# Kernel optimization log

Hardware: AMD Instinct MI355X
Metric: run time of the kernel (lower is better)

The kernel has to match this reference:

```python
import jax, jax.numpy as jnp
from jax import lax
import numpy as np

B, N = 64, 128           # graphs per batch, nodes per graph
MAX_LEVEL = 3
N_TRUNKS, TRUNK_LEN = 32, 32
H, OUT = 256, 10


def setup_inputs() -> dict:
    key = jax.random.key(0)
    ks = jax.random.split(key, 12)
    batch_feature = jax.random.normal(ks[0], (B, N), dtype=jnp.float32)
    trunk_idx = jax.random.randint(ks[1], (MAX_LEVEL, N_TRUNKS, TRUNK_LEN), 0, N, dtype=jnp.int32)
    trunk_len = jax.random.randint(ks[2], (MAX_LEVEL, N_TRUNKS), 1, TRUNK_LEN + 1, dtype=jnp.int32)
    s = 1.0 / np.sqrt(H)
    W_enc = jax.random.uniform(ks[3], (1, H), jnp.float32, -1.0, 1.0)
    b_enc = jax.random.uniform(ks[4], (H,), jnp.float32, -1.0, 1.0)
    W_ih = jax.random.uniform(ks[5], (MAX_LEVEL, 4 * H, H), jnp.float32, -s, s)
    W_hh = jax.random.uniform(ks[6], (MAX_LEVEL, 4 * H, H), jnp.float32, -s, s)
    b_ih = jax.random.uniform(ks[7], (MAX_LEVEL, 4 * H), jnp.float32, -s, s)
    b_hh = jax.random.uniform(ks[8], (MAX_LEVEL, 4 * H), jnp.float32, -s, s)
    W_lin = jax.random.uniform(ks[9], (MAX_LEVEL, H, OUT), jnp.float32, -s, s)
    b_lin = jax.random.uniform(ks[10], (MAX_LEVEL, OUT), jnp.float32, -s, s)
    return {"batch_feature": batch_feature, "trunk_idx": trunk_idx, "trunk_len": trunk_len,
            "W_enc": W_enc, "b_enc": b_enc, "W_ih": W_ih, "W_hh": W_hh,
            "b_ih": b_ih, "b_hh": b_hh, "W_lin": W_lin, "b_lin": b_lin}


def _lstm_scan(seq, W_ih, W_hh, b):
    """seq: [L, M, H] -> all hidden states [L, M, H] (single-layer LSTM, PyTorch gate order i,f,g,o)."""
    M = seq.shape[1]
    Hd = W_hh.shape[1]
    def step(carry, x_t):
        h, c = carry
        gates = x_t @ W_ih.T + h @ W_hh.T + b   # [M, 4H]
        i, f, g, o = jnp.split(gates, 4, axis=-1)
        c = jax.nn.sigmoid(f) * c + jax.nn.sigmoid(i) * jnp.tanh(g)
        h = jax.nn.sigmoid(o) * jnp.tanh(c)
        return (h, c), h
    init = (jnp.zeros((M, Hd), seq.dtype), jnp.zeros((M, Hd), seq.dtype))
    _, hs = lax.scan(step, init, seq)
    return hs


def reference(batch_feature, trunk_idx, trunk_len, W_enc, b_enc, W_ih, W_hh, b_ih, b_hh, W_lin, b_lin):
    Bv, Nv = batch_feature.shape
    Hd = W_enc.shape[1]
    # node encoder on scalar features: x [B*N, 1] @ W_enc [1, H]
    x_attr = (batch_feature.reshape(-1, 1) @ W_enc + b_enc).reshape(Bv, Nv, Hd)
    trunk_len = jnp.maximum(trunk_len, 1)
    score = jnp.zeros((Bv, W_lin.shape[-1]), x_attr.dtype)
    for l in range(trunk_idx.shape[0]):
        idx = trunk_idx[l]                       # [T, L]
        T, L = idx.shape
        seqs = x_attr[:, idx]                    # gather trunks -> [B, T, L, H]
        seqs = seqs.reshape(Bv * T, L, Hd).transpose(1, 0, 2)   # [L, B*T, H]
        hs = _lstm_scan(seqs, W_ih[l], W_hh[l], b_ih[l] + b_hh[l])  # [L, B*T, H]
        lens = jnp.tile(trunk_len[l], Bv)        # [B*T]
        h_last = hs[lens - 1, jnp.arange(Bv * T)]   # hidden at last valid step (== packed h_n)
        h_trunk = h_last.reshape(Bv, T, Hd).sum(axis=1)  # scatter-sum per graph (indices are i repeated T times)
        score = score + h_trunk @ W_lin[l] + b_lin[l]
    return score


if __name__ == "__main__":
    out = reference(**setup_inputs())
    print(out.shape, out.dtype)
```

## Files before the change

kernel.cpp:

```cpp
#include <hip/hip_runtime.h>
#include <hip/hip_bf16.h>
#include <stdint.h>

#define B_   64
#define N_   128
#define H_   256
#define FH   1024
#define NT   32
#define TL   32
#define LV   3
#define OUT_ 10
#define NTRK 96
#define UNITS 384

typedef __attribute__((ext_vector_type(4))) int   int4v;
typedef __attribute__((ext_vector_type(4))) float f32x4;

#define QW  (0.0625f / 127.0f)
#define QH  (1.0f / 127.0f)
#define QS  (QW * QH)
#define L2E 1.442695041f
#define QSI (-L2E * QS)
#define QSG (2.0f * L2E * QS)
#define C2  (2.0f * L2E)

__device__ inline float exp2f_(float x) { return __builtin_amdgcn_exp2f(x); }
__device__ inline float rcpf_(float x)  { return __builtin_amdgcn_rcpf(x); }

__global__ void prep_all(const float* __restrict__ W_enc, const float* __restrict__ b_enc,
                         const float* __restrict__ W_ih, const float* __restrict__ b_ih,
                         const float* __restrict__ b_hh, const float* __restrict__ W_hh,
                         const float* __restrict__ b_lin, const int* __restrict__ trunk_len,
                         float* __restrict__ u, float* __restrict__ v,
                         char* __restrict__ whh_i8, float* __restrict__ out,
                         int* __restrict__ sorted, int* __restrict__ counter) {
    int blk = blockIdx.x;
    int tid = threadIdx.x;
    if (blk < 768) {
        int j = blk * 4 + (tid >> 6);
        int lane = tid & 63;
        const float4 w  = ((const float4*)(W_ih + (size_t)j * H_))[lane];
        const float4 we = ((const float4*)W_enc)[lane];
        const float4 be = ((const float4*)b_enc)[lane];
        float du = w.x * we.x + w.y * we.y + w.z * we.z + w.w * we.w;
        float dv = w.x * be.x + w.y * be.y + w.z * be.z + w.w * be.w;
        for (int m = 32; m >= 1; m >>= 1) { du += __shfl_xor(du, m); dv += __shfl_xor(dv, m); }
        if (lane == 0) {
            int g = (j & 1023) >> 8;
            float s = (g == 2) ? (2.0f * L2E) : (-L2E);
            u[j] = s * du;
            v[j] = s * (dv + b_ih[j] + b_hh[j]);
        }
    } else if (blk < 1536) {
        int gid = (blk - 768) * 256 + tid;
        const float4 w = ((const float4*)W_hh)[gid];
        char4 o;
        int a0 = __float2int_rn(w.x * (127.0f / 0.0625f));
        int a1 = __float2int_rn(w.y * (127.0f / 0.0625f));
        int a2 = __float2int_rn(w.z * (127.0f / 0.0625f));
        int a3 = __float2int_rn(w.w * (127.0f / 0.0625f));
        a0 = a0 > 127 ? 127 : (a0 < -127 ? -127 : a0);
        a1 = a1 > 127 ? 127 : (a1 < -127 ? -127 : a1);
        a2 = a2 > 127 ? 127 : (a2 < -127 ? -127 : a2);
        a3 = a3 > 127 ? 127 : (a3 < -127 ? -127 : a3);
        o.x = (char)a0; o.y = (char)a1; o.z = (char)a2; o.w = (char)a3;
        ((char4*)whh_i8)[gid] = o;
        if (gid < B_ * OUT_) {
            int oo = gid % OUT_;
            out[gid] = b_lin[oo] + b_lin[OUT_ + oo] + b_lin[2 * OUT_ + oo];
        }
    } else {
        if (tid < NTRK) {
            int li = trunk_len[tid]; if (li < 1) li = 1;
            int rank = 0;
            for (int j2 = 0; j2 < NTRK; ++j2) {
                int lj = trunk_len[j2]; if (lj < 1) lj = 1;
                rank += (lj > li) || (lj == li && j2 < tid);
            }
            sorted[rank] = tid;
        }
        if (tid == 0) *counter = 0;
    }
}

__global__ __launch_bounds__(1024) __attribute__((amdgpu_waves_per_eu(4, 4)))
void lstm_main(const float* __restrict__ bfeat, const int* __restrict__ trunk_idx,
               const int* __restrict__ trunk_len,
               const char* __restrict__ whh_i8,
               const float* __restrict__ u, const float* __restrict__ v,
               const float* __restrict__ W_lin, const int* __restrict__ sorted,
               int* __restrict__ counter, float* __restrict__ out) {
    __shared__ __align__(16) char hbuf[2][16][272];
    __shared__ __align__(16) float sbuf[2][16];
    __shared__ int sh_uid;

    const int tid = threadIdx.x;
    const int w = tid >> 6;
    const int lane = tid & 63;
    const int col = lane & 15;
    const int q = lane >> 4;

    int4v z4; z4[0] = 0; z4[1] = 0; z4[2] = 0; z4[3] = 0;
    asm volatile("" : "+v"(z4));

    for (;;) {
        if (tid == 0) sh_uid = atomicAdd(counter, 1);
        __syncthreads();
        const int uid = sh_uid;
        if (uid >= UNITS) break;

        const int r = uid >> 2, qq = uid & 3;
        const int tt = sorted[r];
        const int l = tt >> 5;
        const int b0 = qq * 16;

        int len = trunk_len[tt];
        if (len < 1) len = 1;
        const int* tix = trunk_idx + tt * TL;
        const char* whh_l = whh_i8 + (size_t)l * FH * H_;

        int4v Breg[4][4];
        #pragma unroll
        for (int g = 0; g < 4; ++g) {
            int j = g * 256 + w * 16 + col;
            const char* bp = whh_l + (size_t)j * H_ + q * 16;
            #pragma unroll
            for (int k = 0; k < 4; ++k)
                Breg[g][k] = *(const int4v*)(bp + k * 64);
        }

        float u_r[4], v_r[4];
        {
            const float* u_l = u + l * FH;
            const float* v_l = v + l * FH;
            #pragma unroll
            for (int g = 0; g < 4; ++g) {
                int j = g * 256 + w * 16 + col;
                u_r[g] = u_l[j];
                v_r[g] = v_l[j];
            }
        }

        #pragma unroll
        for (int g = 0; g < 4; ++g) {
            #pragma unroll
            for (int k = 0; k < 4; ++k)
                asm volatile("" : "+v"(Breg[g][k]));
            asm volatile("" : "+v"(u_r[g]), "+v"(v_r[g]));
        }

        float c_r[4];

        if (tid < 16) sbuf[0][tid] = bfeat[(b0 + tid) * N_ + tix[0]];
        __syncthreads();

        {
            if (len > 1 && tid < 16) sbuf[1][tid] = bfeat[(b0 + tid) * N_ + tix[1]];
            f32x4 sv = *(const f32x4*)&sbuf[0][q * 4];
            #pragma unroll
            for (int rg = 0; rg < 4; ++rg) {
                float xi = fmaf(sv[rg], u_r[0], v_r[0]);
                float xg = fmaf(sv[rg], u_r[2], v_r[2]);
                float xo = fmaf(sv[rg], u_r[3], v_r[3]);
                float si = rcpf_(exp2f_(xi) + 1.0f);
                float so = rcpf_(exp2f_(xo) + 1.0f);
                float tg = fmaf(-2.0f, rcpf_(exp2f_(xg) + 1.0f), 1.0f);
                float cn = si * tg;
                c_r[rg] = cn;
                float th127 = fmaf(-254.0f, rcpf_(exp2f_(C2 * cn) + 1.0f), 127.0f);
                hbuf[1][q * 4 + rg][w * 16 + col] = (char)__float2int_rn(so * th127);
            }
            __syncthreads();
        }

        for (int p = 1; p < len; ++p) {
            const int ri = p & 1, wi = ri ^ 1;

            if (p + 1 < len && tid < 16)
                sbuf[wi][tid] = bfeat[(b0 + tid) * N_ + tix[p + 1]];

            f32x4 sv = *(const f32x4*)&sbuf[ri][q * 4];

            int4v acc[4];
            #pragma unroll
            for (int k = 0; k < 4; ++k) {
                int4v af = *(const int4v*)&hbuf[ri][col][k * 64 + q * 16];
                if (k == 0) {
                    #pragma unroll
                    for (int g = 0; g < 4; ++g)
                        acc[g] = __builtin_amdgcn_mfma_i32_16x16x64_i8(af, Breg[g][0], z4, 0, 0, 0);
                } else {
                    #pragma unroll
                    for (int g = 0; g < 4; ++g)
                        acc[g] = __builtin_amdgcn_mfma_i32_16x16x64_i8(af, Breg[g][k], acc[g], 0, 0, 0);
                }
            }

            #pragma unroll
            for (int rg = 0; rg < 4; ++rg) {
                float xi = fmaf((float)acc[0][rg], QSI, fmaf(sv[rg], u_r[0], v_r[0]));
                float xf = fmaf((float)acc[1][rg], QSI, fmaf(sv[rg], u_r[1], v_r[1]));
                float xg = fmaf((float)acc[2][rg], QSG, fmaf(sv[rg], u_r[2], v_r[2]));
                float xo = fmaf((float)acc[3][rg], QSI, fmaf(sv[rg], u_r[3], v_r[3]));
                float si = rcpf_(exp2f_(xi) + 1.0f);
                float sf = rcpf_(exp2f_(xf) + 1.0f);
                float so = rcpf_(exp2f_(xo) + 1.0f);
                float tg = fmaf(-2.0f, rcpf_(exp2f_(xg) + 1.0f), 1.0f);
                float cn = fmaf(sf, c_r[rg], si * tg);
                c_r[rg] = cn;
                float th127 = fmaf(-254.0f, rcpf_(exp2f_(C2 * cn) + 1.0f), 127.0f);
                hbuf[wi][q * 4 + rg][w * 16 + col] = (char)__float2int_rn(so * th127);
            }

            __syncthreads();
        }

        const char (*hl)[272] = hbuf[len & 1];
        const float* wl = W_lin + l * H_ * OUT_;
        if (tid < 16 * OUT_) {
            int m = tid / OUT_, o = tid % OUT_;
            float s = 0.f;
            for (int k = 0; k < H_; ++k)
                s += (float)hl[m][k] * QH * wl[k * OUT_ + o];
            atomicAdd(&out[(b0 + m) * OUT_ + o], s);
        }
    }
}

extern "C" void kernel_launch(void* const* d_in, const int* in_sizes, int n_in,
                              void* d_out, int out_size, void* d_ws, size_t ws_size,
                              hipStream_t stream) {
    const float* bfeat = (const float*)d_in[0];
    const int*   tidx  = (const int*)d_in[1];
    const int*   tlen  = (const int*)d_in[2];
    const float* W_enc = (const float*)d_in[3];
    const float* b_enc = (const float*)d_in[4];
    const float* W_ih  = (const float*)d_in[5];
    const float* W_hh  = (const float*)d_in[6];
    const float* b_ih  = (const float*)d_in[7];
    const float* b_hh  = (const float*)d_in[8];
    const float* W_lin = (const float*)d_in[9];
    const float* b_lin = (const float*)d_in[10];
    float* out = (float*)d_out;

    char*  whh_i8 = (char*)d_ws;
    float* u = (float*)((char*)d_ws + 786432);
    float* v = (float*)((char*)d_ws + 786432 + 12288);
    int* sorted  = (int*)((char*)d_ws + 811008);
    int* counter = (int*)((char*)d_ws + 811392);

    prep_all<<<1537, 256, 0, stream>>>(W_enc, b_enc, W_ih, b_ih, b_hh, W_hh, b_lin,
                                       tlen, u, v, whh_i8, out, sorted, counter);
    lstm_main<<<256, 1024, 0, stream>>>(bfeat, tidx, tlen, whh_i8, u, v, W_lin,
                                        sorted, counter, out);
}
```

Baseline: 149.2 us.

## Fuse prep kernel into LSTM kernel using a grid-wide barrier

Folds the weight-preparation kernel (u/v projections, int8 quantization of W_hh, output bias init, trunk sorting) into the persistent LSTM kernel. All 256 blocks do a slice of the prep work and then meet at an atomic grid barrier before the LSTM loop. The counter and barrier are zeroed with a memset instead. This removes one kernel launch and the gap between kernels. The cost is a memset call plus a spin barrier, which relies on all 256 blocks being co-resident.

```diff
diff --git a/kernel.cpp b/kernel.cpp
--- a/kernel.cpp
+++ b/kernel.cpp
@@ -12,6 +12,7 @@
 #define OUT_ 10
 #define NTRK 96
 #define UNITS 384
+#define NBLK 256
 
 typedef __attribute__((ext_vector_type(4))) int   int4v;
 typedef __attribute__((ext_vector_type(4))) float f32x4;
@@ -27,23 +28,33 @@
 __device__ inline float exp2f_(float x) { return __builtin_amdgcn_exp2f(x); }
 __device__ inline float rcpf_(float x)  { return __builtin_amdgcn_rcpf(x); }
 
-__global__ void prep_all(const float* __restrict__ W_enc, const float* __restrict__ b_enc,
-                         const float* __restrict__ W_ih, const float* __restrict__ b_ih,
-                         const float* __restrict__ b_hh, const float* __restrict__ W_hh,
-                         const float* __restrict__ b_lin, const int* __restrict__ trunk_len,
-                         float* __restrict__ u, float* __restrict__ v,
-                         char* __restrict__ whh_i8, float* __restrict__ out,
-                         int* __restrict__ sorted, int* __restrict__ counter) {
-    int blk = blockIdx.x;
-    int tid = threadIdx.x;
-    if (blk < 768) {
-        int j = blk * 4 + (tid >> 6);
-        int lane = tid & 63;
-        const float4 w  = ((const float4*)(W_ih + (size_t)j * H_))[lane];
+__global__ __launch_bounds__(1024) __attribute__((amdgpu_waves_per_eu(4, 4)))
+void lstm_fused(const float* __restrict__ bfeat, const int* __restrict__ trunk_idx,
+                const int* __restrict__ trunk_len,
+                const float* __restrict__ W_enc, const float* __restrict__ b_enc,
+                const float* __restrict__ W_ih, const float* __restrict__ b_ih,
+                const float* __restrict__ b_hh, const float* __restrict__ W_hh,
+                const float* __restrict__ W_lin, const float* __restrict__ b_lin,
+                char* __restrict__ whh_i8, float* __restrict__ u, float* __restrict__ v,
+                int* __restrict__ sorted, int* __restrict__ counter,
+                int* __restrict__ gbar, float* __restrict__ out) {
+    __shared__ __align__(16) char hbuf[2][16][272];
+    __shared__ __align__(16) float sbuf[2][16];
+    __shared__ int sh_uid;
+
+    const int tid = threadIdx.x;
+    const int w = tid >> 6;
+    const int lane = tid & 63;
+    const int col = lane & 15;
+    const int q = lane >> 4;
+
+    if (w < 12) {
+        int j = blockIdx.x * 12 + w;
+        const float4 wv = ((const float4*)(W_ih + (size_t)j * H_))[lane];
         const float4 we = ((const float4*)W_enc)[lane];
         const float4 be = ((const float4*)b_enc)[lane];
-        float du = w.x * we.x + w.y * we.y + w.z * we.z + w.w * we.w;
-        float dv = w.x * be.x + w.y * be.y + w.z * be.z + w.w * be.w;
+        float du = wv.x * we.x + wv.y * we.y + wv.z * we.z + wv.w * we.w;
+        float dv = wv.x * be.x + wv.y * be.y + wv.z * be.z + wv.w * be.w;
         for (int m = 32; m >= 1; m >>= 1) { du += __shfl_xor(du, m); dv += __shfl_xor(dv, m); }
         if (lane == 0) {
             int g = (j & 1023) >> 8;
@@ -51,25 +62,27 @@
             u[j] = s * du;
             v[j] = s * (dv + b_ih[j] + b_hh[j]);
         }
-    } else if (blk < 1536) {
-        int gid = (blk - 768) * 256 + tid;
-        const float4 w = ((const float4*)W_hh)[gid];
+    }
+    if (tid < 768) {
+        int gid = blockIdx.x * 768 + tid;
+        const float4 wv = ((const float4*)W_hh)[gid];
         char4 o;
-        int a0 = __float2int_rn(w.x * (127.0f / 0.0625f));
-        int a1 = __float2int_rn(w.y * (127.0f / 0.0625f));
-        int a2 = __float2int_rn(w.z * (127.0f / 0.0625f));
-        int a3 = __float2int_rn(w.w * (127.0f / 0.0625f));
+        int a0 = __float2int_rn(wv.x * (127.0f / 0.0625f));
+        int a1 = __float2int_rn(wv.y * (127.0f / 0.0625f));
+        int a2 = __float2int_rn(wv.z * (127.0f / 0.0625f));
+        int a3 = __float2int_rn(wv.w * (127.0f / 0.0625f));
         a0 = a0 > 127 ? 127 : (a0 < -127 ? -127 : a0);
         a1 = a1 > 127 ? 127 : (a1 < -127 ? -127 : a1);
         a2 = a2 > 127 ? 127 : (a2 < -127 ? -127 : a2);
         a3 = a3 > 127 ? 127 : (a3 < -127 ? -127 : a3);
         o.x = (char)a0; o.y = (char)a1; o.z = (char)a2; o.w = (char)a3;
         ((char4*)whh_i8)[gid] = o;
-        if (gid < B_ * OUT_) {
-            int oo = gid % OUT_;
-            out[gid] = b_lin[oo] + b_lin[OUT_ + oo] + b_lin[2 * OUT_ + oo];
-        }
-    } else {
+    }
+    if (blockIdx.x == 0) {
+        if (tid < B_ * OUT_) {
+            int oo = tid % OUT_;
+            out[tid] = b_lin[oo] + b_lin[OUT_ + oo] + b_lin[2 * OUT_ + oo];
+        }
         if (tid < NTRK) {
             int li = trunk_len[tid]; if (li < 1) li = 1;
             int rank = 0;
@@ -79,26 +92,17 @@
             }
             sorted[rank] = tid;
         }
-        if (tid == 0) *counter = 0;
-    }
-}
-
-__global__ __launch_bounds__(1024) __attribute__((amdgpu_waves_per_eu(4, 4)))
-void lstm_main(const float* __restrict__ bfeat, const int* __restrict__ trunk_idx,
-               const int* __restrict__ trunk_len,
-               const char* __restrict__ whh_i8,
-               const float* __restrict__ u, const float* __restrict__ v,
-               const float* __restrict__ W_lin, const int* __restrict__ sorted,
-               int* __restrict__ counter, float* __restrict__ out) {
-    __shared__ __align__(16) char hbuf[2][16][272];
-    __shared__ __align__(16) float sbuf[2][16];
-    __shared__ int sh_uid;
-
-    const int tid = threadIdx.x;
-    const int w = tid >> 6;
-    const int lane = tid & 63;
-    const int col = lane & 15;
-    const int q = lane >> 4;
+    }
+
+    __syncthreads();
+    if (tid == 0) {
+        __threadfence();
+        atomicAdd(gbar, 1);
+        while (__hip_atomic_load(gbar, __ATOMIC_ACQUIRE, __HIP_MEMORY_SCOPE_AGENT) < NBLK)
+            __builtin_amdgcn_s_sleep(2);
+    }
+    __syncthreads();
+    __threadfence();
 
     int4v z4; z4[0] = 0; z4[1] = 0; z4[2] = 0; z4[3] = 0;
     asm volatile("" : "+v"(z4));
@@ -248,9 +252,11 @@
     float* v = (float*)((char*)d_ws + 786432 + 12288);
     int* sorted  = (int*)((char*)d_ws + 811008);
     int* counter = (int*)((char*)d_ws + 811392);
-
-    prep_all<<<1537, 256, 0, stream>>>(W_enc, b_enc, W_ih, b_ih, b_hh, W_hh, b_lin,
-                                       tlen, u, v, whh_i8, out, sorted, counter);
-    lstm_main<<<256, 1024, 0, stream>>>(bfeat, tidx, tlen, whh_i8, u, v, W_lin,
-                                        sorted, counter, out);
+    int* gbar    = (int*)((char*)d_ws + 811396);
+
+    hipMemsetAsync((char*)d_ws + 811392, 0, 8, stream);
+
+    lstm_fused<<<NBLK, 1024, 0, stream>>>(bfeat, tidx, tlen, W_enc, b_enc, W_ih,
+                                          b_ih, b_hh, W_hh, W_lin, b_lin,
+                                          whh_i8, u, v, sorted, counter, gbar, out);
 }
```

Result: slower. 223.9 us (+50.1%).

## Process 32 batch rows per work unit to halve unit count and reuse weights

Applied to the files above, without the earlier changes.

Each work unit now covers 32 graphs of a trunk instead of 16, so there are half as many units and each block loads its int8 W_hh fragments into registers once for twice the rows. Two independent MFMA accumulator chains (A and B halves) are interleaved per step, which gives the matrix units more independent work per barrier. The cost is doubled per-step elementwise gate work per thread, more registers, and coarser load balancing across the persistent blocks, since a long trunk now occupies a block for twice the rows.

```diff
diff --git a/kernel.cpp b/kernel.cpp
--- a/kernel.cpp
+++ b/kernel.cpp
@@ -11,7 +11,7 @@
 #define LV   3
 #define OUT_ 10
 #define NTRK 96
-#define UNITS 384
+#define UNITS 192
 
 typedef __attribute__((ext_vector_type(4))) int   int4v;
 typedef __attribute__((ext_vector_type(4))) float f32x4;
@@ -90,8 +90,8 @@
                const float* __restrict__ u, const float* __restrict__ v,
                const float* __restrict__ W_lin, const int* __restrict__ sorted,
                int* __restrict__ counter, float* __restrict__ out) {
-    __shared__ __align__(16) char hbuf[2][16][272];
-    __shared__ __align__(16) float sbuf[2][16];
+    __shared__ __align__(16) char hbuf[2][32][272];
+    __shared__ __align__(16) float sbuf[2][32];
     __shared__ int sh_uid;
 
     const int tid = threadIdx.x;
@@ -109,10 +109,9 @@
         const int uid = sh_uid;
         if (uid >= UNITS) break;
 
-        const int r = uid >> 2, qq = uid & 3;
-        const int tt = sorted[r];
+        const int tt = sorted[uid >> 1];
         const int l = tt >> 5;
-        const int b0 = qq * 16;
+        const int b0 = (uid & 1) * 32;
 
         int len = trunk_len[tt];
         if (len < 1) len = 1;
@@ -149,26 +148,41 @@
             asm volatile("" : "+v"(u_r[g]), "+v"(v_r[g]));
         }
 
-        float c_r[4];
-
-        if (tid < 16) sbuf[0][tid] = bfeat[(b0 + tid) * N_ + tix[0]];
+        float cA[4], cB[4];
+
+        if (tid < 32) sbuf[0][tid] = bfeat[(b0 + tid) * N_ + tix[0]];
         __syncthreads();
 
         {
-            if (len > 1 && tid < 16) sbuf[1][tid] = bfeat[(b0 + tid) * N_ + tix[1]];
-            f32x4 sv = *(const f32x4*)&sbuf[0][q * 4];
+            if (len > 1 && tid < 32) sbuf[1][tid] = bfeat[(b0 + tid) * N_ + tix[1]];
+            f32x4 svA = *(const f32x4*)&sbuf[0][q * 4];
+            f32x4 svB = *(const f32x4*)&sbuf[0][16 + q * 4];
             #pragma unroll
             for (int rg = 0; rg < 4; ++rg) {
-                float xi = fmaf(sv[rg], u_r[0], v_r[0]);
-                float xg = fmaf(sv[rg], u_r[2], v_r[2]);
-                float xo = fmaf(sv[rg], u_r[3], v_r[3]);
-                float si = rcpf_(exp2f_(xi) + 1.0f);
-                float so = rcpf_(exp2f_(xo) + 1.0f);
-                float tg = fmaf(-2.0f, rcpf_(exp2f_(xg) + 1.0f), 1.0f);
-                float cn = si * tg;
-                c_r[rg] = cn;
-                float th127 = fmaf(-254.0f, rcpf_(exp2f_(C2 * cn) + 1.0f), 127.0f);
-                hbuf[1][q * 4 + rg][w * 16 + col] = (char)__float2int_rn(so * th127);
+                {
+                    float xi = fmaf(svA[rg], u_r[0], v_r[0]);
+                    float xg = fmaf(svA[rg], u_r[2], v_r[2]);
+                    float xo = fmaf(svA[rg], u_r[3], v_r[3]);
+                    float si = rcpf_(exp2f_(xi) + 1.0f);
+                    float so = rcpf_(exp2f_(xo) + 1.0f);
+                    float tg = fmaf(-2.0f, rcpf_(exp2f_(xg) + 1.0f), 1.0f);
+                    float cn = si * tg;
+                    cA[rg] = cn;
+                    float th127 = fmaf(-254.0f, rcpf_(exp2f_(C2 * cn) + 1.0f), 127.0f);
+                    hbuf[1][q * 4 + rg][w * 16 + col] = (char)__float2int_rn(so * th127);
+                }
+                {
+                    float xi = fmaf(svB[rg], u_r[0], v_r[0]);
+                    float xg = fmaf(svB[rg], u_r[2], v_r[2]);
+                    float xo = fmaf(svB[rg], u_r[3], v_r[3]);
+                    float si = rcpf_(exp2f_(xi) + 1.0f);
+                    float so = rcpf_(exp2f_(xo) + 1.0f);
+                    float tg = fmaf(-2.0f, rcpf_(exp2f_(xg) + 1.0f), 1.0f);
+                    float cn = si * tg;
+                    cB[rg] = cn;
+                    float th127 = fmaf(-254.0f, rcpf_(exp2f_(C2 * cn) + 1.0f), 127.0f);
+                    hbuf[1][16 + q * 4 + rg][w * 16 + col] = (char)__float2int_rn(so * th127);
+                }
             }
             __syncthreads();
         }
@@ -176,40 +190,62 @@
         for (int p = 1; p < len; ++p) {
             const int ri = p & 1, wi = ri ^ 1;
 
-            if (p + 1 < len && tid < 16)
+            if (p + 1 < len && tid < 32)
                 sbuf[wi][tid] = bfeat[(b0 + tid) * N_ + tix[p + 1]];
 
-            f32x4 sv = *(const f32x4*)&sbuf[ri][q * 4];
-
-            int4v acc[4];
+            f32x4 svA = *(const f32x4*)&sbuf[ri][q * 4];
+            f32x4 svB = *(const f32x4*)&sbuf[ri][16 + q * 4];
+
+            int4v accA[4], accB[4];
             #pragma unroll
             for (int k = 0; k < 4; ++k) {
-                int4v af = *(const int4v*)&hbuf[ri][col][k * 64 + q * 16];
+                int4v afA = *(const int4v*)&hbuf[ri][col][k * 64 + q * 16];
+                int4v afB = *(const int4v*)&hbuf[ri][16 + col][k * 64 + q * 16];
                 if (k == 0) {
                     #pragma unroll
-                    for (int g = 0; g < 4; ++g)
-                        acc[g] = __builtin_amdgcn_mfma_i32_16x16x64_i8(af, Breg[g][0], z4, 0, 0, 0);
+                    for (int g = 0; g < 4; ++g) {
+                        accA[g] = __builtin_amdgcn_mfma_i32_16x16x64_i8(afA, Breg[g][0], z4, 0, 0, 0);
+                        accB[g] = __builtin_amdgcn_mfma_i32_16x16x64_i8(afB, Breg[g][0], z4, 0, 0, 0);
+                    }
                 } else {
                     #pragma unroll
-                    for (int g = 0; g < 4; ++g)
-                        acc[g] = __builtin_amdgcn_mfma_i32_16x16x64_i8(af, Breg[g][k], acc[g], 0, 0, 0);
+                    for (int g = 0; g < 4; ++g) {
+                        accA[g] = __builtin_amdgcn_mfma_i32_16x16x64_i8(afA, Breg[g][k], accA[g], 0, 0, 0);
+                        accB[g] = __builtin_amdgcn_mfma_i32_16x16x64_i8(afB, Breg[g][k], accB[g], 0, 0, 0);
+                    }
                 }
             }
 
             #pragma unroll
             for (int rg = 0; rg < 4; ++rg) {
-                float xi = fmaf((float)acc[0][rg], QSI, fmaf(sv[rg], u_r[0], v_r[0]));
-                float xf = fmaf((float)acc[1][rg], QSI, fmaf(sv[rg], u_r[1], v_r[1]));
-                float xg = fmaf((float)acc[2][rg], QSG, fmaf(sv[rg], u_r[2], v_r[2]));
-                float xo = fmaf((float)acc[3][rg], QSI, fmaf(sv[rg], u_r[3], v_r[3]));
-                float si = rcpf_(exp2f_(xi) + 1.0f);
-                float sf = rcpf_(exp2f_(xf) + 1.0f);
-                float so = rcpf_(exp2f_(xo) + 1.0f);
-                float tg = fmaf(-2.0f, rcpf_(exp2f_(xg) + 1.0f), 1.0f);
-                float cn = fmaf(sf, c_r[rg], si * tg);
-                c_r[rg] = cn;
-                float th127 = fmaf(-254.0f, rcpf_(exp2f_(C2 * cn) + 1.0f), 127.0f);
-                hbuf[wi][q * 4 + rg][w * 16 + col] = (char)__float2int_rn(so * th127);
+                {
+                    float xi = fmaf((float)accA[0][rg], QSI, fmaf(svA[rg], u_r[0], v_r[0]));
+                    float xf = fmaf((float)accA[1][rg], QSI, fmaf(svA[rg], u_r[1], v_r[1]));
+                    float xg = fmaf((float)accA[2][rg], QSG, fmaf(svA[rg], u_r[2], v_r[2]));
+                    float xo = fmaf((float)accA[3][rg], QSI, fmaf(svA[rg], u_r[3], v_r[3]));
+                    float si = rcpf_(exp2f_(xi) + 1.0f);
+                    float sf = rcpf_(exp2f_(xf) + 1.0f);
+                    float so = rcpf_(exp2f_(xo) + 1.0f);
+                    float tg = fmaf(-2.0f, rcpf_(exp2f_(xg) + 1.0f), 1.0f);
+                    float cn = fmaf(sf, cA[rg], si * tg);
+                    cA[rg] = cn;
+                    float th127 = fmaf(-254.0f, rcpf_(exp2f_(C2 * cn) + 1.0f), 127.0f);
+                    hbuf[wi][q * 4 + rg][w * 16 + col] = (char)__float2int_rn(so * th127);
+                }
+                {
+                    float xi = fmaf((float)accB[0][rg], QSI, fmaf(svB[rg], u_r[0], v_r[0]));
+                    float xf = fmaf((float)accB[1][rg], QSI, fmaf(svB[rg], u_r[1], v_r[1]));
+                    float xg = fmaf((float)accB[2][rg], QSG, fmaf(svB[rg], u_r[2], v_r[2]));
+                    float xo = fmaf((float)accB[3][rg], QSI, fmaf(svB[rg], u_r[3], v_r[3]));
+                    float si = rcpf_(exp2f_(xi) + 1.0f);
+                    float sf = rcpf_(exp2f_(xf) + 1.0f);
+                    float so = rcpf_(exp2f_(xo) + 1.0f);
+                    float tg = fmaf(-2.0f, rcpf_(exp2f_(xg) + 1.0f), 1.0f);
+                    float cn = fmaf(sf, cB[rg], si * tg);
+                    cB[rg] = cn;
+                    float th127 = fmaf(-254.0f, rcpf_(exp2f_(C2 * cn) + 1.0f), 127.0f);
+                    hbuf[wi][16 + q * 4 + rg][w * 16 + col] = (char)__float2int_rn(so * th127);
+                }
             }
 
             __syncthreads();
@@ -217,7 +253,7 @@
 
         const char (*hl)[272] = hbuf[len & 1];
         const float* wl = W_lin + l * H_ * OUT_;
-        if (tid < 16 * OUT_) {
+        if (tid < 32 * OUT_) {
             int m = tid / OUT_, o = tid % OUT_;
             float s = 0.f;
             for (int k = 0; k < H_; ++k)
```

After: 250.2 us. +67.7%, slower.
